# Kernel optimization log

Hardware: AMD Instinct MI355X
Metric: run time of the kernel (lower is better)

Reference implementation:

```python
import jax, jax.numpy as jnp
import numpy as np

# dims: T tokens, H hidden, E experts, I expert intermediate, K top-k
T, H, E, I, K = 2048, 1024, 64, 768, 8


def setup_inputs() -> dict:
    key = jax.random.key(0)
    k0, k1, k2, k3, k4 = jax.random.split(key, 5)
    s = 0.02  # init scale
    return {
        "hidden_states": jax.random.normal(k0, (T, H), jnp.float32),
        "w_router": jax.random.normal(k1, (E, H), jnp.float32) * s,   # gate (router) Linear, no bias
        "w_gate": jax.random.normal(k2, (E, I, H), jnp.float32) * s,  # per-expert gate_proj (out,in)
        "w_up": jax.random.normal(k3, (E, I, H), jnp.float32) * s,    # per-expert up_proj
        "w_down": jax.random.normal(k4, (E, H, I), jnp.float32) * s,  # per-expert down_proj
    }


def reference(hidden_states, w_router, w_gate, w_up, w_down):
    x = hidden_states  # (T, H)
    # --- router: softmax scores, top-k selection, renormalize (select_experts, softmax scoring) ---
    router_logits = jnp.einsum("th,eh->te", x, w_router)          # (T, E)
    probs = jax.nn.softmax(router_logits, axis=-1)
    topk_w, topk_ids = jax.lax.top_k(probs, K)                     # (T, K)
    topk_w = topk_w / jnp.sum(topk_w, axis=-1, keepdims=True)      # renormalize=True
    # scatter per-slot weights into a (T, E) combine matrix (zero for unselected experts)
    route = jnp.zeros((x.shape[0], E), x.dtype)
    route = route.at[jnp.arange(x.shape[0])[:, None], topk_ids].add(topk_w)
    # --- experts: SwiGLU MLP per expert, weighted combine (FusedMoE dispatch/combine) ---
    g = jnp.einsum("th,eih->tei", x, w_gate)                       # (T, E, I)
    u = jnp.einsum("th,eih->tei", x, w_up)
    h = jax.nn.silu(g) * u
    y = jnp.einsum("tei,ehi,te->th", h, w_down, route)             # weighted scatter-combine
    return y
```

## Files before the change

kernel.cpp:

```cpp
#include <hip/hip_runtime.h>
#include <hip/hip_bf16.h>
#include <cstdint>
#include <cstddef>

#define T_TOK 2048
#define H_DIM 1024
#define E_NUM 64
#define I_DIM 768
#define K_TOP 8
#define BM 384

typedef __attribute__((ext_vector_type(8))) __bf16 bf16x8;
typedef __attribute__((ext_vector_type(4))) __bf16 bf16x4;
typedef __attribute__((ext_vector_type(8))) unsigned short u16x8;
typedef __attribute__((ext_vector_type(4))) float f32x4;
typedef unsigned short ushort_t;

__device__ __forceinline__ unsigned short f2bf(float f) {
  uint32_t u = __builtin_bit_cast(uint32_t, f);
  u += 0x7fffu + ((u >> 16) & 1u);
  return (unsigned short)(u >> 16);
}

__device__ __forceinline__ bf16x8 cvt8b(f32x4 a, f32x4 b) {
  bf16x8 r;
  r[0] = (__bf16)a[0]; r[1] = (__bf16)a[1]; r[2] = (__bf16)a[2]; r[3] = (__bf16)a[3];
  r[4] = (__bf16)b[0]; r[5] = (__bf16)b[1]; r[6] = (__bf16)b[2]; r[7] = (__bf16)b[3];
  return r;
}

__device__ __forceinline__ bf16x4 cvt4b(f32x4 a) {
  bf16x4 r;
  r[0] = (__bf16)a[0]; r[1] = (__bf16)a[1]; r[2] = (__bf16)a[2]; r[3] = (__bf16)a[3];
  return r;
}

__device__ __forceinline__ void async16(const void* l, const void* g) {
  __builtin_amdgcn_global_load_lds(
      (const __attribute__((address_space(1))) unsigned int*)g,
      (__attribute__((address_space(3))) unsigned int*)l, 16, 0, 0);
}

__global__ __launch_bounds__(256) void xcast_kernel(const float* __restrict__ x,
                                                    ushort_t* __restrict__ xb) {
  int i = blockIdx.x * 256 + threadIdx.x;
  const f32x4* s = (const f32x4*)(x + (size_t)i * 8);
  *(bf16x8*)(xb + (size_t)i * 8) = cvt8b(s[0], s[1]);
}

__global__ __launch_bounds__(64) void router_kernel(
    const float* __restrict__ x, const float* __restrict__ wr,
    int* __restrict__ topk_id, float* __restrict__ topk_w,
    int* __restrict__ counts) {
  const int t0 = blockIdx.x * 4;
  const int e = threadIdx.x;
  const float4* wv = (const float4*)(wr + (size_t)e * H_DIM);
  const float4* xv0 = (const float4*)(x + (size_t)t0 * H_DIM);
  const float4* xv1 = (const float4*)(x + (size_t)(t0 + 1) * H_DIM);
  const float4* xv2 = (const float4*)(x + (size_t)(t0 + 2) * H_DIM);
  const float4* xv3 = (const float4*)(x + (size_t)(t0 + 3) * H_DIM);
  float acc0 = 0.f, acc1 = 0.f, acc2 = 0.f, acc3 = 0.f;
#pragma unroll 4
  for (int i = 0; i < H_DIM / 4; ++i) {
    float4 b = wv[i];
    float4 a0 = xv0[i], a1 = xv1[i], a2 = xv2[i], a3 = xv3[i];
    acc0 = fmaf(a0.x, b.x, fmaf(a0.y, b.y, fmaf(a0.z, b.z, fmaf(a0.w, b.w, acc0))));
    acc1 = fmaf(a1.x, b.x, fmaf(a1.y, b.y, fmaf(a1.z, b.z, fmaf(a1.w, b.w, acc1))));
    acc2 = fmaf(a2.x, b.x, fmaf(a2.y, b.y, fmaf(a2.z, b.z, fmaf(a2.w, b.w, acc2))));
    acc3 = fmaf(a3.x, b.x, fmaf(a3.y, b.y, fmaf(a3.z, b.z, fmaf(a3.w, b.w, acc3))));
  }
  float accs[4] = {acc0, acc1, acc2, acc3};
#pragma unroll 1
  for (int tt = 0; tt < 4; ++tt) {
    int t = t0 + tt;
    float acc = accs[tt];
    float m = acc;
    for (int o = 32; o; o >>= 1) m = fmaxf(m, __shfl_xor(m, o));
    float p = __expf(acc - m);
    float s = p;
    for (int o = 32; o; o >>= 1) s += __shfl_xor(s, o);
    p /= s;
    float v = p;
    int sid = 0;
    float sw = 0.f;
    for (int k = 0; k < K_TOP; ++k) {
      float bv = v;
      int bi = e;
      for (int o = 32; o; o >>= 1) {
        float ov = __shfl_xor(bv, o);
        int oi = __shfl_xor(bi, o);
        if (ov > bv || (ov == bv && oi < bi)) { bv = ov; bi = oi; }
      }
      if (e == k) { sid = bi; sw = bv; }
      if (e == bi) v = -1.f;
    }
    float ssum = (e < K_TOP) ? sw : 0.f;
    for (int o = 32; o; o >>= 1) ssum += __shfl_xor(ssum, o);
    if (e < K_TOP) {
      topk_id[t * K_TOP + e] = sid;
      topk_w[t * K_TOP + e] = sw / ssum;
      atomicAdd(&counts[sid], 1);
    }
  }
}

__global__ __launch_bounds__(64) void scan_kernel(
    const int* __restrict__ counts, int* __restrict__ offsets,
    int* __restrict__ cursor) {
  int e = threadIdx.x;
  int ne = counts[e];
  int x = ne;
  for (int o = 1; o < 64; o <<= 1) {
    int v = __shfl_up(x, o);
    if (e >= o) x += v;
  }
  int excl = x - ne;
  offsets[e] = excl;
  cursor[e] = excl;
}

__global__ __launch_bounds__(256) void build_kernel(
    const int* __restrict__ topk_id, const float* __restrict__ topk_w,
    int* __restrict__ cursor, int* __restrict__ pair_token, float* __restrict__ pair_w) {
  int i = blockIdx.x * 256 + threadIdx.x;
  int t = i >> 3;
  int e = topk_id[i];
  int pos = atomicAdd(&cursor[e], 1);
  pair_token[pos] = t;
  pair_w[pos] = topk_w[i];
}


#define GU_NIT 32

__global__ __launch_bounds__(768, 3) void gemm_gu_kernel(
    const ushort_t* __restrict__ xb, const float* __restrict__ wg,
    const float* __restrict__ wu, const int* __restrict__ offsets,
    const int* __restrict__ counts, const int* __restrict__ pair_token,
    ushort_t* __restrict__ h_buf) {
  int idx = (blockIdx.x & 7) * 96 + (blockIdx.x >> 3);
  int e = idx / 12, nt = idx - e * 12;
  int ne = counts[e], off = offsets[e];
  int ib = nt * 64;

  __shared__ __align__(16) ushort_t Xs[2][BM * 32];
  __shared__ __align__(16) ushort_t Gs[2][64 * 32];
  __shared__ __align__(16) ushort_t Us[2][64 * 32];
  __shared__ int sTok[BM];

  const int tid = threadIdx.x;
  const int lane = tid & 63;
  const int wid = tid >> 6;
  if (tid < BM) {
    sTok[tid] = pair_token[off + (tid < ne ? tid : ne - 1)];
  }
  __syncthreads();

  const ushort_t* xsrc[2];
#pragma unroll
  for (int j = 0; j < 2; ++j) {
    int p = j * 768 + tid;
    int row = p >> 2, c = p & 3;
    xsrc[j] = xb + (size_t)sTok[row] * H_DIM + ((c ^ ((row >> 1) & 3)) << 3);
  }
  const float* gsrc = wg;
  const float* usrc = wu;
  int wdsti = 0;
  if (wid < 8) {
    int wrow = tid >> 3, wq = tid & 7;
    size_t ro = ((size_t)e * I_DIM + ib + wrow) * H_DIM + wq * 4;
    gsrc = wg + ro;
    usrc = wu + ro;
    wdsti = wrow * 32 + (((wq >> 1) ^ ((wrow >> 1) & 3)) << 3) + ((wq & 1) << 2);
  }

  const int wrM = wid >> 1, wrN = wid & 1;
  const int lrow = lane & 15, lk = lane >> 4;
  const bool wact = (wrM * 64) < ne;

  f32x4 accG[4][2], accU[4][2];
#pragma unroll
  for (int mi = 0; mi < 4; ++mi)
#pragma unroll
    for (int ni = 0; ni < 2; ++ni) {
      accG[mi][ni] = f32x4{0.f, 0.f, 0.f, 0.f};
      accU[mi][ni] = f32x4{0.f, 0.f, 0.f, 0.f};
    }

  f32x4 gA = {0, 0, 0, 0}, uA = {0, 0, 0, 0};

#define GU_XDMA(B, K0)                                             \
  do {                                                             \
    async16(&Xs[B][(wid * 64) * 8], xsrc[0] + (K0));               \
    async16(&Xs[B][(768 + wid * 64) * 8], xsrc[1] + (K0));         \
  } while (0)

  GU_XDMA(0, 0);
  if (wid < 8) {
    gA = *(const f32x4*)(gsrc);
    uA = *(const f32x4*)(usrc);
  }
  asm volatile("s_waitcnt vmcnt(0)" ::: "memory");
  __builtin_amdgcn_sched_barrier(0);
  if (wid < 8) {
    *(bf16x4*)&Gs[0][wdsti] = cvt4b(gA);
    *(bf16x4*)&Us[0][wdsti] = cvt4b(uA);
  }
  asm volatile("s_waitcnt lgkmcnt(0)" ::: "memory");
  __builtin_amdgcn_s_barrier();
  __builtin_amdgcn_sched_barrier(0);

#pragma unroll 2
  for (int K = 0; K < GU_NIT; ++K) {
    const int B = K & 1;
    if (K + 1 < GU_NIT) {
      GU_XDMA(B ^ 1, (K + 1) * 32);
      if (wid < 8) {
        gA = *(const f32x4*)(gsrc + (K + 1) * 32);
        uA = *(const f32x4*)(usrc + (K + 1) * 32);
      }
    }
    if (wact) {
      __builtin_amdgcn_s_setprio(1);
      bf16x8 af[4];
#pragma unroll
      for (int mi = 0; mi < 4; ++mi) {
        int r = wrM * 64 + mi * 16 + lrow;
        af[mi] = __builtin_bit_cast(
            bf16x8, *(const u16x8*)&Xs[B][r * 32 + ((lk ^ ((r >> 1) & 3)) << 3)]);
      }
#pragma unroll
      for (int ni = 0; ni < 2; ++ni) {
        int br = wrN * 32 + ni * 16 + lrow;
        int ci = br * 32 + ((lk ^ ((br >> 1) & 3)) << 3);
        bf16x8 bg = __builtin_bit_cast(bf16x8, *(const u16x8*)&Gs[B][ci]);
        bf16x8 bu = __builtin_bit_cast(bf16x8, *(const u16x8*)&Us[B][ci]);
#pragma unroll
        for (int mi = 0; mi < 4; ++mi) {
          accG[mi][ni] = __builtin_amdgcn_mfma_f32_16x16x32_bf16(af[mi], bg, accG[mi][ni], 0, 0, 0);
          accU[mi][ni] = __builtin_amdgcn_mfma_f32_16x16x32_bf16(af[mi], bu, accU[mi][ni], 0, 0, 0);
        }
      }
      __builtin_amdgcn_s_setprio(0);
    }
    asm volatile("s_waitcnt vmcnt(0)" ::: "memory");
    __builtin_amdgcn_sched_barrier(0);
    if (K + 1 < GU_NIT && wid < 8) {
      *(bf16x4*)&Gs[B ^ 1][wdsti] = cvt4b(gA);
      *(bf16x4*)&Us[B ^ 1][wdsti] = cvt4b(uA);
    }
    asm volatile("s_waitcnt lgkmcnt(0)" ::: "memory");
    __builtin_amdgcn_s_barrier();
    __builtin_amdgcn_sched_barrier(0);
  }
#undef GU_XDMA

#pragma unroll
  for (int mi = 0; mi < 4; ++mi)
#pragma unroll
    for (int ni = 0; ni < 2; ++ni)
#pragma unroll
      for (int r = 0; r < 4; ++r) {
        int grow = wrM * 64 + mi * 16 + lk * 4 + r;
        if (grow < ne) {
          int col = ib + wrN * 32 + ni * 16 + lrow;
          float g = accG[mi][ni][r], u = accU[mi][ni][r];
          float hv = g / (1.f + __expf(-g)) * u;
          h_buf[(size_t)(off + grow) * I_DIM + col] = f2bf(hv);
        }
      }
}

#define DN_NIT 24

__global__ __launch_bounds__(768, 3) void gemm_down_kernel(
    const ushort_t* __restrict__ h_buf, const float* __restrict__ wd,
    const int* __restrict__ offsets, const int* __restrict__ counts,
    const int* __restrict__ pair_token, const float* __restrict__ pair_w,
    float* __restrict__ y) {
  int idx = (blockIdx.x & 7) * 64 + (blockIdx.x >> 3);
  int e = idx >> 3, nt = idx & 7;
  int ne = counts[e], off = offsets[e];
  int hb = nt * 128;

  __shared__ __align__(16) ushort_t Ah[2][BM * 32];
  __shared__ __align__(16) ushort_t Bs[2][128 * 32];
  __shared__ int sTok[BM];
  __shared__ float sPw[BM];

  const int tid = threadIdx.x;
  const int lane = tid & 63;
  const int wid = tid >> 6;
  if (tid < BM) {
    int ix = off + (tid < ne ? tid : ne - 1);
    sTok[tid] = pair_token[ix];
    sPw[tid] = pair_w[ix];
  }
  __syncthreads();

  const ushort_t* asrc[2];
#pragma unroll
  for (int j = 0; j < 2; ++j) {
    int p = j * 768 + tid;
    int row = p >> 2, c = p & 3;
    int hr = off + (row < ne ? row : ne - 1);
    asrc[j] = h_buf + (size_t)hr * I_DIM + ((c ^ ((row >> 1) & 3)) << 3);
  }
  const float* bsrc0 = wd;
  const float* bsrc1 = wd;
  int bdst0 = 0, bdst1 = 0;
  if (wid < 8) {
    int r0 = tid >> 3, q0 = tid & 7;
    bsrc0 = wd + ((size_t)e * H_DIM + hb + r0) * I_DIM + q0 * 4;
    bdst0 = r0 * 32 + (((q0 >> 1) ^ ((r0 >> 1) & 3)) << 3) + ((q0 & 1) << 2);
    int p1 = 512 + tid;
    int r1 = p1 >> 3, q1 = p1 & 7;
    bsrc1 = wd + ((size_t)e * H_DIM + hb + r1) * I_DIM + q1 * 4;
    bdst1 = r1 * 32 + (((q1 >> 1) ^ ((r1 >> 1) & 3)) << 3) + ((q1 & 1) << 2);
  }

  const int wrM = wid >> 1, wrN = wid & 1;
  const int lrow = lane & 15, lk = lane >> 4;
  const bool wact = (wrM * 64) < ne;

  f32x4 acc[4][4];
#pragma unroll
  for (int mi = 0; mi < 4; ++mi)
#pragma unroll
    for (int ni = 0; ni < 4; ++ni) acc[mi][ni] = f32x4{0.f, 0.f, 0.f, 0.f};

  f32x4 bA = {0, 0, 0, 0}, bB = {0, 0, 0, 0};

#define DN_ADMA(B, K0)                                             \
  do {                                                             \
    async16(&Ah[B][(wid * 64) * 8], asrc[0] + (K0));               \
    async16(&Ah[B][(768 + wid * 64) * 8], asrc[1] + (K0));         \
  } while (0)

  DN_ADMA(0, 0);
  if (wid < 8) {
    bA = *(const f32x4*)(bsrc0);
    bB = *(const f32x4*)(bsrc1);
  }
  asm volatile("s_waitcnt vmcnt(0)" ::: "memory");
  __builtin_amdgcn_sched_barrier(0);
  if (wid < 8) {
    *(bf16x4*)&Bs[0][bdst0] = cvt4b(bA);
    *(bf16x4*)&Bs[0][bdst1] = cvt4b(bB);
  }
  asm volatile("s_waitcnt lgkmcnt(0)" ::: "memory");
  __builtin_amdgcn_s_barrier();
  __builtin_amdgcn_sched_barrier(0);

#pragma unroll 2
  for (int K = 0; K < DN_NIT; ++K) {
    const int B = K & 1;
    if (K + 1 < DN_NIT) {
      DN_ADMA(B ^ 1, (K + 1) * 32);
      if (wid < 8) {
        bA = *(const f32x4*)(bsrc0 + (K + 1) * 32);
        bB = *(const f32x4*)(bsrc1 + (K + 1) * 32);
      }
    }
    if (wact) {
      __builtin_amdgcn_s_setprio(1);
      bf16x8 af[4];
#pragma unroll
      for (int mi = 0; mi < 4; ++mi) {
        int r = wrM * 64 + mi * 16 + lrow;
        af[mi] = __builtin_bit_cast(
            bf16x8, *(const u16x8*)&Ah[B][r * 32 + ((lk ^ ((r >> 1) & 3)) << 3)]);
      }
#pragma unroll
      for (int ni = 0; ni < 4; ++ni) {
        int br = wrN * 64 + ni * 16 + lrow;
        bf16x8 bb = __builtin_bit_cast(
            bf16x8, *(const u16x8*)&Bs[B][br * 32 + ((lk ^ ((br >> 1) & 3)) << 3)]);
#pragma unroll
        for (int mi = 0; mi < 4; ++mi)
          acc[mi][ni] = __builtin_amdgcn_mfma_f32_16x16x32_bf16(af[mi], bb, acc[mi][ni], 0, 0, 0);
      }
      __builtin_amdgcn_s_setprio(0);
    }
    asm volatile("s_waitcnt vmcnt(0)" ::: "memory");
    __builtin_amdgcn_sched_barrier(0);
    if (K + 1 < DN_NIT && wid < 8) {
      *(bf16x4*)&Bs[B ^ 1][bdst0] = cvt4b(bA);
      *(bf16x4*)&Bs[B ^ 1][bdst1] = cvt4b(bB);
    }
    asm volatile("s_waitcnt lgkmcnt(0)" ::: "memory");
    __builtin_amdgcn_s_barrier();
    __builtin_amdgcn_sched_barrier(0);
  }
#undef DN_ADMA

#pragma unroll
  for (int mi = 0; mi < 4; ++mi)
#pragma unroll
    for (int ni = 0; ni < 4; ++ni)
#pragma unroll
      for (int r = 0; r < 4; ++r) {
        int grow = wrM * 64 + mi * 16 + lk * 4 + r;
        if (grow < ne) {
          int col = hb + wrN * 64 + ni * 16 + lrow;
          float val = acc[mi][ni][r] * sPw[grow];
          unsafeAtomicAdd(&y[(size_t)sTok[grow] * H_DIM + col], val);
        }
      }
}

extern "C" void kernel_launch(void* const* d_in, const int* in_sizes, int n_in,
                              void* d_out, int out_size, void* d_ws, size_t ws_size,
                              hipStream_t stream) {
  const float* x  = (const float*)d_in[0];
  const float* wr = (const float*)d_in[1];
  const float* wg = (const float*)d_in[2];
  const float* wu = (const float*)d_in[3];
  const float* wd = (const float*)d_in[4];
  float* y = (float*)d_out;

  char* ws = (char*)d_ws;
  int* counts    = (int*)(ws + 0);
  int* offsets   = (int*)(ws + 256);
  int* cursor    = (int*)(ws + 512);
  int*   topk_id    = (int*)(ws + 2048);
  float* topk_w     = (float*)(ws + 2048 + 1 * 65536);
  int*   pair_token = (int*)(ws + 2048 + 2 * 65536);
  float* pair_w     = (float*)(ws + 2048 + 3 * 65536);
  ushort_t* h_buf = (ushort_t*)(ws + 2048 + 4 * 65536);
  ushort_t* xb = (ushort_t*)(ws + 2048 + 4 * 65536 + (size_t)T_TOK * I_DIM * K_TOP * 2);

  hipMemsetAsync(counts, 0, 256, stream);
  hipMemsetAsync(y, 0, (size_t)T_TOK * H_DIM * sizeof(float), stream);

  xcast_kernel<<<(T_TOK * H_DIM / 8) / 256, 256, 0, stream>>>(x, xb);
  router_kernel<<<T_TOK / 4, 64, 0, stream>>>(x, wr, topk_id, topk_w, counts);
  scan_kernel<<<1, 64, 0, stream>>>(counts, offsets, cursor);
  build_kernel<<<(T_TOK * K_TOP) / 256, 256, 0, stream>>>(topk_id, topk_w, cursor, pair_token, pair_w);
  gemm_gu_kernel<<<768, 768, 0, stream>>>(
      xb, wg, wu, offsets, counts, pair_token, h_buf);
  gemm_down_kernel<<<512, 768, 0, stream>>>(
      h_buf, wd, offsets, counts, pair_token, pair_w, y);
}
```

Before: 372.7 us.

## Split expert GEMMs into 128-row tiles via a tile list with XCD-aware mapping

The scan kernel now builds a compact list of (expert, 128-row sub-tile) entries, and both expert GEMMs launch 256-thread blocks that each handle one 128-row tile instead of 768-thread blocks covering up to 384 rows. Block indices are remapped so consecutive tiles land on the same XCD, and blocks with no valid tile exit early. The aim is to cut wasted idle waves on lightly loaded experts and improve load balance across CUs. In exchange, the double-buffered software pipeline is replaced by a single buffer with two syncthreads per iteration, and the fp32 weight tile is re-read by every row tile of an expert, which may raise memory traffic unless L2 absorbs it.

```diff
diff --git a/kernel.cpp b/kernel.cpp
--- a/kernel.cpp
+++ b/kernel.cpp
@@ -8,10 +8,8 @@
 #define E_NUM 64
 #define I_DIM 768
 #define K_TOP 8
-#define BM 384
 
 typedef __attribute__((ext_vector_type(8))) __bf16 bf16x8;
-typedef __attribute__((ext_vector_type(4))) __bf16 bf16x4;
 typedef __attribute__((ext_vector_type(8))) unsigned short u16x8;
 typedef __attribute__((ext_vector_type(4))) float f32x4;
 typedef unsigned short ushort_t;
@@ -22,17 +20,11 @@
   return (unsigned short)(u >> 16);
 }
 
-__device__ __forceinline__ bf16x8 cvt8b(f32x4 a, f32x4 b) {
+__device__ __forceinline__ u16x8 cvt8b(f32x4 a, f32x4 b) {
   bf16x8 r;
   r[0] = (__bf16)a[0]; r[1] = (__bf16)a[1]; r[2] = (__bf16)a[2]; r[3] = (__bf16)a[3];
   r[4] = (__bf16)b[0]; r[5] = (__bf16)b[1]; r[6] = (__bf16)b[2]; r[7] = (__bf16)b[3];
-  return r;
-}
-
-__device__ __forceinline__ bf16x4 cvt4b(f32x4 a) {
-  bf16x4 r;
-  r[0] = (__bf16)a[0]; r[1] = (__bf16)a[1]; r[2] = (__bf16)a[2]; r[3] = (__bf16)a[3];
-  return r;
+  return __builtin_bit_cast(u16x8, r);
 }
 
 __device__ __forceinline__ void async16(const void* l, const void* g) {
@@ -41,11 +33,19 @@
       (__attribute__((address_space(3))) unsigned int*)l, 16, 0, 0);
 }
 
+__device__ __forceinline__ int xcd_decode(int wg0, int n_act) {
+  int q = n_act >> 3, r = n_act & 7;
+  int xcd = wg0 & 7, rank = wg0 >> 3;
+  int cnt = q + (xcd < r ? 1 : 0);
+  if (rank >= cnt) return -1;
+  return (xcd < r ? xcd * (q + 1) : r * (q + 1) + (xcd - r) * q) + rank;
+}
+
 __global__ __launch_bounds__(256) void xcast_kernel(const float* __restrict__ x,
                                                     ushort_t* __restrict__ xb) {
   int i = blockIdx.x * 256 + threadIdx.x;
   const f32x4* s = (const f32x4*)(x + (size_t)i * 8);
-  *(bf16x8*)(xb + (size_t)i * 8) = cvt8b(s[0], s[1]);
+  *(u16x8*)(xb + (size_t)i * 8) = cvt8b(s[0], s[1]);
 }
 
 __global__ __launch_bounds__(64) void router_kernel(
@@ -106,7 +106,8 @@
 
 __global__ __launch_bounds__(64) void scan_kernel(
     const int* __restrict__ counts, int* __restrict__ offsets,
-    int* __restrict__ cursor) {
+    int* __restrict__ cursor, int* __restrict__ tile_list,
+    int* __restrict__ n_tiles) {
   int e = threadIdx.x;
   int ne = counts[e];
   int x = ne;
@@ -117,6 +118,16 @@
   int excl = x - ne;
   offsets[e] = excl;
   cursor[e] = excl;
+  int ntl = (ne + 127) >> 7;
+  if (ntl > 3) ntl = 3;
+  int y2 = ntl;
+  for (int o = 1; o < 64; o <<= 1) {
+    int v = __shfl_up(y2, o);
+    if (e >= o) y2 += v;
+  }
+  int texcl = y2 - ntl;
+  for (int m = 0; m < ntl; ++m) tile_list[texcl + m] = (e << 2) | m;
+  if (e == 63) *n_tiles = texcl + ntl;
 }
 
 __global__ __launch_bounds__(256) void build_kernel(
@@ -133,50 +144,54 @@
 
 #define GU_NIT 32
 
-__global__ __launch_bounds__(768, 3) void gemm_gu_kernel(
+__global__ __launch_bounds__(256, 3) void gemm_gu_kernel(
     const ushort_t* __restrict__ xb, const float* __restrict__ wg,
     const float* __restrict__ wu, const int* __restrict__ offsets,
     const int* __restrict__ counts, const int* __restrict__ pair_token,
+    const int* __restrict__ tile_list, const int* __restrict__ n_tiles,
     ushort_t* __restrict__ h_buf) {
-  int idx = (blockIdx.x & 7) * 96 + (blockIdx.x >> 3);
-  int e = idx / 12, nt = idx - e * 12;
+  int idx = xcd_decode(blockIdx.x, (*n_tiles) * 12);
+  if (idx < 0) return;
+  int tl = idx / 12, nt = idx - tl * 12;
+  int ent = tile_list[tl];
+  int e = ent >> 2, mt = ent & 3;
   int ne = counts[e], off = offsets[e];
   int ib = nt * 64;
-
-  __shared__ __align__(16) ushort_t Xs[2][BM * 32];
-  __shared__ __align__(16) ushort_t Gs[2][64 * 32];
-  __shared__ __align__(16) ushort_t Us[2][64 * 32];
-  __shared__ int sTok[BM];
+  int vr = ne - mt * 128;
+  if (vr <= 0) return;
+  if (vr > 128) vr = 128;
+
+  __shared__ __align__(16) ushort_t Xs[128 * 32];
+  __shared__ __align__(16) ushort_t Gs[64 * 32];
+  __shared__ __align__(16) ushort_t Us[64 * 32];
+  __shared__ int sTok[128];
 
   const int tid = threadIdx.x;
   const int lane = tid & 63;
   const int wid = tid >> 6;
-  if (tid < BM) {
-    sTok[tid] = pair_token[off + (tid < ne ? tid : ne - 1)];
+  if (tid < 128) {
+    int p = mt * 128 + tid;
+    sTok[tid] = pair_token[off + (p < ne ? p : ne - 1)];
   }
   __syncthreads();
 
   const ushort_t* xsrc[2];
+  int xdst[2];
 #pragma unroll
   for (int j = 0; j < 2; ++j) {
-    int p = j * 768 + tid;
+    int p = j * 256 + tid;
     int row = p >> 2, c = p & 3;
     xsrc[j] = xb + (size_t)sTok[row] * H_DIM + ((c ^ ((row >> 1) & 3)) << 3);
-  }
-  const float* gsrc = wg;
-  const float* usrc = wu;
-  int wdsti = 0;
-  if (wid < 8) {
-    int wrow = tid >> 3, wq = tid & 7;
-    size_t ro = ((size_t)e * I_DIM + ib + wrow) * H_DIM + wq * 4;
-    gsrc = wg + ro;
-    usrc = wu + ro;
-    wdsti = wrow * 32 + (((wq >> 1) ^ ((wrow >> 1) & 3)) << 3) + ((wq & 1) << 2);
-  }
+    xdst[j] = (j * 256 + wid * 64) * 8;
+  }
+  const int wrow = tid >> 2, wc = tid & 3;
+  const float* gsrc = wg + ((size_t)e * I_DIM + ib + wrow) * H_DIM + wc * 8;
+  const float* usrc = wu + ((size_t)e * I_DIM + ib + wrow) * H_DIM + wc * 8;
+  const int wdst = (wrow * 4 + (wc ^ ((wrow >> 1) & 3))) * 8;
 
   const int wrM = wid >> 1, wrN = wid & 1;
   const int lrow = lane & 15, lk = lane >> 4;
-  const bool wact = (wrM * 64) < ne;
+  const bool wact = (wrM * 64) < vr;
 
   f32x4 accG[4][2], accU[4][2];
 #pragma unroll
@@ -187,73 +202,43 @@
       accU[mi][ni] = f32x4{0.f, 0.f, 0.f, 0.f};
     }
 
-  f32x4 gA = {0, 0, 0, 0}, uA = {0, 0, 0, 0};
-
-#define GU_XDMA(B, K0)                                             \
-  do {                                                             \
-    async16(&Xs[B][(wid * 64) * 8], xsrc[0] + (K0));               \
-    async16(&Xs[B][(768 + wid * 64) * 8], xsrc[1] + (K0));         \
-  } while (0)
-
-  GU_XDMA(0, 0);
-  if (wid < 8) {
-    gA = *(const f32x4*)(gsrc);
-    uA = *(const f32x4*)(usrc);
-  }
-  asm volatile("s_waitcnt vmcnt(0)" ::: "memory");
-  __builtin_amdgcn_sched_barrier(0);
-  if (wid < 8) {
-    *(bf16x4*)&Gs[0][wdsti] = cvt4b(gA);
-    *(bf16x4*)&Us[0][wdsti] = cvt4b(uA);
-  }
-  asm volatile("s_waitcnt lgkmcnt(0)" ::: "memory");
-  __builtin_amdgcn_s_barrier();
-  __builtin_amdgcn_sched_barrier(0);
-
-#pragma unroll 2
-  for (int K = 0; K < GU_NIT; ++K) {
-    const int B = K & 1;
-    if (K + 1 < GU_NIT) {
-      GU_XDMA(B ^ 1, (K + 1) * 32);
-      if (wid < 8) {
-        gA = *(const f32x4*)(gsrc + (K + 1) * 32);
-        uA = *(const f32x4*)(usrc + (K + 1) * 32);
-      }
-    }
+#pragma unroll 1
+  for (int k = 0; k < GU_NIT; ++k) {
+    const int k0 = k * 32;
+    async16(&Xs[xdst[0]], xsrc[0] + k0);
+    async16(&Xs[xdst[1]], xsrc[1] + k0);
+    {
+      f32x4 g0 = *(const f32x4*)(gsrc + k0);
+      f32x4 g1 = *(const f32x4*)(gsrc + k0 + 4);
+      f32x4 u0 = *(const f32x4*)(usrc + k0);
+      f32x4 u1 = *(const f32x4*)(usrc + k0 + 4);
+      *(u16x8*)&Gs[wdst] = cvt8b(g0, g1);
+      *(u16x8*)&Us[wdst] = cvt8b(u0, u1);
+    }
+    __syncthreads();
     if (wact) {
-      __builtin_amdgcn_s_setprio(1);
       bf16x8 af[4];
 #pragma unroll
       for (int mi = 0; mi < 4; ++mi) {
         int r = wrM * 64 + mi * 16 + lrow;
         af[mi] = __builtin_bit_cast(
-            bf16x8, *(const u16x8*)&Xs[B][r * 32 + ((lk ^ ((r >> 1) & 3)) << 3)]);
+            bf16x8, *(const u16x8*)&Xs[r * 32 + ((lk ^ ((r >> 1) & 3)) << 3)]);
       }
 #pragma unroll
       for (int ni = 0; ni < 2; ++ni) {
         int br = wrN * 32 + ni * 16 + lrow;
         int ci = br * 32 + ((lk ^ ((br >> 1) & 3)) << 3);
-        bf16x8 bg = __builtin_bit_cast(bf16x8, *(const u16x8*)&Gs[B][ci]);
-        bf16x8 bu = __builtin_bit_cast(bf16x8, *(const u16x8*)&Us[B][ci]);
+        bf16x8 bg = __builtin_bit_cast(bf16x8, *(const u16x8*)&Gs[ci]);
+        bf16x8 bu = __builtin_bit_cast(bf16x8, *(const u16x8*)&Us[ci]);
 #pragma unroll
         for (int mi = 0; mi < 4; ++mi) {
           accG[mi][ni] = __builtin_amdgcn_mfma_f32_16x16x32_bf16(af[mi], bg, accG[mi][ni], 0, 0, 0);
           accU[mi][ni] = __builtin_amdgcn_mfma_f32_16x16x32_bf16(af[mi], bu, accU[mi][ni], 0, 0, 0);
         }
       }
-      __builtin_amdgcn_s_setprio(0);
-    }
-    asm volatile("s_waitcnt vmcnt(0)" ::: "memory");
-    __builtin_amdgcn_sched_barrier(0);
-    if (K + 1 < GU_NIT && wid < 8) {
-      *(bf16x4*)&Gs[B ^ 1][wdsti] = cvt4b(gA);
-      *(bf16x4*)&Us[B ^ 1][wdsti] = cvt4b(uA);
-    }
-    asm volatile("s_waitcnt lgkmcnt(0)" ::: "memory");
-    __builtin_amdgcn_s_barrier();
-    __builtin_amdgcn_sched_barrier(0);
-  }
-#undef GU_XDMA
+    }
+    __syncthreads();
+  }
 
 #pragma unroll
   for (int mi = 0; mi < 4; ++mi)
@@ -262,66 +247,69 @@
 #pragma unroll
       for (int r = 0; r < 4; ++r) {
         int grow = wrM * 64 + mi * 16 + lk * 4 + r;
-        if (grow < ne) {
+        if (grow < vr) {
           int col = ib + wrN * 32 + ni * 16 + lrow;
           float g = accG[mi][ni][r], u = accU[mi][ni][r];
           float hv = g / (1.f + __expf(-g)) * u;
-          h_buf[(size_t)(off + grow) * I_DIM + col] = f2bf(hv);
+          h_buf[(size_t)(off + mt * 128 + grow) * I_DIM + col] = f2bf(hv);
         }
       }
 }
 
 #define DN_NIT 24
 
-__global__ __launch_bounds__(768, 3) void gemm_down_kernel(
+__global__ __launch_bounds__(256, 3) void gemm_down_kernel(
     const ushort_t* __restrict__ h_buf, const float* __restrict__ wd,
     const int* __restrict__ offsets, const int* __restrict__ counts,
     const int* __restrict__ pair_token, const float* __restrict__ pair_w,
+    const int* __restrict__ tile_list, const int* __restrict__ n_tiles,
     float* __restrict__ y) {
-  int idx = (blockIdx.x & 7) * 64 + (blockIdx.x >> 3);
-  int e = idx >> 3, nt = idx & 7;
+  int idx = xcd_decode(blockIdx.x, (*n_tiles) * 8);
+  if (idx < 0) return;
+  int tl = idx >> 3, nt = idx & 7;
+  int ent = tile_list[tl];
+  int e = ent >> 2, mt = ent & 3;
   int ne = counts[e], off = offsets[e];
   int hb = nt * 128;
-
-  __shared__ __align__(16) ushort_t Ah[2][BM * 32];
-  __shared__ __align__(16) ushort_t Bs[2][128 * 32];
-  __shared__ int sTok[BM];
-  __shared__ float sPw[BM];
+  int vr = ne - mt * 128;
+  if (vr <= 0) return;
+  if (vr > 128) vr = 128;
+
+  __shared__ __align__(16) ushort_t Ah[128 * 32];
+  __shared__ __align__(16) ushort_t Bs[128 * 32];
+  __shared__ int sTok[128];
+  __shared__ float sPw[128];
 
   const int tid = threadIdx.x;
   const int lane = tid & 63;
   const int wid = tid >> 6;
-  if (tid < BM) {
-    int ix = off + (tid < ne ? tid : ne - 1);
+  if (tid < 128) {
+    int p = mt * 128 + tid;
+    int ix = off + (p < ne ? p : ne - 1);
     sTok[tid] = pair_token[ix];
     sPw[tid] = pair_w[ix];
   }
   __syncthreads();
 
   const ushort_t* asrc[2];
+  int adst[2];
 #pragma unroll
   for (int j = 0; j < 2; ++j) {
-    int p = j * 768 + tid;
+    int p = j * 256 + tid;
     int row = p >> 2, c = p & 3;
-    int hr = off + (row < ne ? row : ne - 1);
+    int pr = mt * 128 + row;
+    int hr = off + (pr < ne ? pr : ne - 1);
     asrc[j] = h_buf + (size_t)hr * I_DIM + ((c ^ ((row >> 1) & 3)) << 3);
-  }
-  const float* bsrc0 = wd;
-  const float* bsrc1 = wd;
-  int bdst0 = 0, bdst1 = 0;
-  if (wid < 8) {
-    int r0 = tid >> 3, q0 = tid & 7;
-    bsrc0 = wd + ((size_t)e * H_DIM + hb + r0) * I_DIM + q0 * 4;
-    bdst0 = r0 * 32 + (((q0 >> 1) ^ ((r0 >> 1) & 3)) << 3) + ((q0 & 1) << 2);
-    int p1 = 512 + tid;
-    int r1 = p1 >> 3, q1 = p1 & 7;
-    bsrc1 = wd + ((size_t)e * H_DIM + hb + r1) * I_DIM + q1 * 4;
-    bdst1 = r1 * 32 + (((q1 >> 1) ^ ((r1 >> 1) & 3)) << 3) + ((q1 & 1) << 2);
-  }
+    adst[j] = (j * 256 + wid * 64) * 8;
+  }
+  const int brow = tid >> 1, bc0 = (tid & 1) * 2, bc1 = bc0 + 1;
+  const float* bsrc = wd + ((size_t)e * H_DIM + hb + brow) * I_DIM + bc0 * 8;
+  const int bdst0 = (brow * 4 + (bc0 ^ ((brow >> 1) & 3))) * 8;
+  const int bdst1 = (brow * 4 + (bc1 ^ ((brow >> 1) & 3))) * 8;
 
   const int wrM = wid >> 1, wrN = wid & 1;
   const int lrow = lane & 15, lk = lane >> 4;
-  const bool wact = (wrM * 64) < ne;
+  const bool wact = (wrM * 64) < vr;
 
   f32x4 acc[4][4];
 #pragma unroll
@@ -329,70 +317,40 @@
 #pragma unroll
     for (int ni = 0; ni < 4; ++ni) acc[mi][ni] = f32x4{0.f, 0.f, 0.f, 0.f};
 
-  f32x4 bA = {0, 0, 0, 0}, bB = {0, 0, 0, 0};
-
-#define DN_ADMA(B, K0)                                             \
-  do {                                                             \
-    async16(&Ah[B][(wid * 64) * 8], asrc[0] + (K0));               \
-    async16(&Ah[B][(768 + wid * 64) * 8], asrc[1] + (K0));         \
-  } while (0)
-
-  DN_ADMA(0, 0);
-  if (wid < 8) {
-    bA = *(const f32x4*)(bsrc0);
-    bB = *(const f32x4*)(bsrc1);
-  }
-  asm volatile("s_waitcnt vmcnt(0)" ::: "memory");
-  __builtin_amdgcn_sched_barrier(0);
-  if (wid < 8) {
-    *(bf16x4*)&Bs[0][bdst0] = cvt4b(bA);
-    *(bf16x4*)&Bs[0][bdst1] = cvt4b(bB);
-  }
-  asm volatile("s_waitcnt lgkmcnt(0)" ::: "memory");
-  __builtin_amdgcn_s_barrier();
-  __builtin_amdgcn_sched_barrier(0);
-
-#pragma unroll 2
-  for (int K = 0; K < DN_NIT; ++K) {
-    const int B = K & 1;
-    if (K + 1 < DN_NIT) {
-      DN_ADMA(B ^ 1, (K + 1) * 32);
-      if (wid < 8) {
-        bA = *(const f32x4*)(bsrc0 + (K + 1) * 32);
-        bB = *(const f32x4*)(bsrc1 + (K + 1) * 32);
-      }
-    }
+#pragma unroll 1
+  for (int k = 0; k < DN_NIT; ++k) {
+    const int k0 = k * 32;
+    async16(&Ah[adst[0]], asrc[0] + k0);
+    async16(&Ah[adst[1]], asrc[1] + k0);
+    {
+      f32x4 b0 = *(const f32x4*)(bsrc + k0);
+      f32x4 b1 = *(const f32x4*)(bsrc + k0 + 4);
+      f32x4 b2 = *(const f32x4*)(bsrc + k0 + 8);
+      f32x4 b3 = *(const f32x4*)(bsrc + k0 + 12);
+      *(u16x8*)&Bs[bdst0] = cvt8b(b0, b1);
+      *(u16x8*)&Bs[bdst1] = cvt8b(b2, b3);
+    }
+    __syncthreads();
     if (wact) {
-      __builtin_amdgcn_s_setprio(1);
       bf16x8 af[4];
 #pragma unroll
       for (int mi = 0; mi < 4; ++mi) {
         int r = wrM * 64 + mi * 16 + lrow;
         af[mi] = __builtin_bit_cast(
-            bf16x8, *(const u16x8*)&Ah[B][r * 32 + ((lk ^ ((r >> 1) & 3)) << 3)]);
+            bf16x8, *(const u16x8*)&Ah[r * 32 + ((lk ^ ((r >> 1) & 3)) << 3)]);
       }
 #pragma unroll
       for (int ni = 0; ni < 4; ++ni) {
         int br = wrN * 64 + ni * 16 + lrow;
         bf16x8 bb = __builtin_bit_cast(
-            bf16x8, *(const u16x8*)&Bs[B][br * 32 + ((lk ^ ((br >> 1) & 3)) << 3)]);
+            bf16x8, *(const u16x8*)&Bs[br * 32 + ((lk ^ ((br >> 1) & 3)) << 3)]);
 #pragma unroll
         for (int mi = 0; mi < 4; ++mi)
           acc[mi][ni] = __builtin_amdgcn_mfma_f32_16x16x32_bf16(af[mi], bb, acc[mi][ni], 0, 0, 0);
       }
-      __builtin_amdgcn_s_setprio(0);
-    }
-    asm volatile("s_waitcnt vmcnt(0)" ::: "memory");
-    __builtin_amdgcn_sched_barrier(0);
-    if (K + 1 < DN_NIT && wid < 8) {
-      *(bf16x4*)&Bs[B ^ 1][bdst0] = cvt4b(bA);
-      *(bf16x4*)&Bs[B ^ 1][bdst1] = cvt4b(bB);
-    }
-    asm volatile("s_waitcnt lgkmcnt(0)" ::: "memory");
-    __builtin_amdgcn_s_barrier();
-    __builtin_amdgcn_sched_barrier(0);
-  }
-#undef DN_ADMA
+    }
+    __syncthreads();
+  }
 
 #pragma unroll
   for (int mi = 0; mi < 4; ++mi)
@@ -401,7 +359,7 @@
 #pragma unroll
       for (int r = 0; r < 4; ++r) {
         int grow = wrM * 64 + mi * 16 + lk * 4 + r;
-        if (grow < ne) {
+        if (grow < vr) {
           int col = hb + wrN * 64 + ni * 16 + lrow;
           float val = acc[mi][ni][r] * sPw[grow];
           unsafeAtomicAdd(&y[(size_t)sTok[grow] * H_DIM + col], val);
@@ -423,6 +381,8 @@
   int* counts    = (int*)(ws + 0);
   int* offsets   = (int*)(ws + 256);
   int* cursor    = (int*)(ws + 512);
+  int* n_tiles   = (int*)(ws + 768);
+  int* tile_list = (int*)(ws + 1024);
   int*   topk_id    = (int*)(ws + 2048);
   float* topk_w     = (float*)(ws + 2048 + 1 * 65536);
   int*   pair_token = (int*)(ws + 2048 + 2 * 65536);
@@ -435,10 +395,10 @@
 
   xcast_kernel<<<(T_TOK * H_DIM / 8) / 256, 256, 0, stream>>>(x, xb);
   router_kernel<<<T_TOK / 4, 64, 0, stream>>>(x, wr, topk_id, topk_w, counts);
-  scan_kernel<<<1, 64, 0, stream>>>(counts, offsets, cursor);
+  scan_kernel<<<1, 64, 0, stream>>>(counts, offsets, cursor, tile_list, n_tiles);
   build_kernel<<<(T_TOK * K_TOP) / 256, 256, 0, stream>>>(topk_id, topk_w, cursor, pair_token, pair_w);
-  gemm_gu_kernel<<<768, 768, 0, stream>>>(
-      xb, wg, wu, offsets, counts, pair_token, h_buf);
-  gemm_down_kernel<<<512, 768, 0, stream>>>(
-      h_buf, wd, offsets, counts, pair_token, pair_w, y);
-}
+  gemm_gu_kernel<<<E_NUM * 3 * 12, 256, 0, stream>>>(
+      xb, wg, wu, offsets, counts, pair_token, tile_list, n_tiles, h_buf);
+  gemm_down_kernel<<<E_NUM * 3 * 8, 256, 0, stream>>>(
+      h_buf, wd, offsets, counts, pair_token, pair_w, tile_list, n_tiles, y);
+}
```

Result: slower. 412.7 us (+10.7%).
